# Kernel optimization log

Measured on AMD Instinct MI355X. Metric: run time of the kernel, lower is better.

Reference implementation:

```python
import jax, jax.numpy as jnp
import numpy as np

EMBED = 512
WINDOW = 64

def setup_inputs() -> dict:
    key = jax.random.key(0)
    ks = jax.random.split(key, 5)
    B, S, E = 4, 4096, EMBED
    s = 1.0 / np.sqrt(E)
    x = jax.random.normal(ks[0], (B, S, E), dtype=jnp.float32)
    W_qkv = jax.random.uniform(ks[1], (E, 3 * E), minval=-s, maxval=s, dtype=jnp.float32)
    b_qkv = jax.random.uniform(ks[2], (3 * E,), minval=-s, maxval=s, dtype=jnp.float32)
    W_out = jax.random.uniform(ks[3], (E, E), minval=-s, maxval=s, dtype=jnp.float32)
    b_out = jax.random.uniform(ks[4], (E,), minval=-s, maxval=s, dtype=jnp.float32)
    return {"x": x, "W_qkv": W_qkv, "b_qkv": b_qkv, "W_out": W_out, "b_out": b_out}

def reference(x, W_qkv, b_qkv, W_out, b_out):
    B, S, E = x.shape
    scale = jnp.sqrt(jnp.asarray(E, dtype=x.dtype))
    qkv = x @ W_qkv + b_qkv                    # [B,S,3E]
    q, k, v = jnp.split(qkv, 3, axis=-1)       # each [B,S,E]
    scores = jnp.einsum('bqe,bke->bqk', q, k) / scale  # [B,S,S]
    pos = jnp.arange(S)
    dist = pos[None, :] - pos[:, None]         # [S,S]
    window_mask = jnp.abs(dist) <= WINDOW
    neg_inf = jnp.asarray(-jnp.inf, dtype=scores.dtype)
    scores = jnp.where(window_mask[None, :, :], scores, neg_inf)
    attn = jax.nn.softmax(scores, axis=-1)     # every row has in-window entries
    attended = jnp.einsum('bqk,bke->bqe', attn, v)
    return attended @ W_out + b_out
```

## Files before the change

### kernel.cpp

```cpp
#include <hip/hip_runtime.h>

typedef __attribute__((ext_vector_type(8))) _Float16 f16x8;
typedef __attribute__((ext_vector_type(4))) _Float16 f16x4;
typedef __attribute__((ext_vector_type(4))) float f32x4;
typedef __attribute__((address_space(1))) const char gc_char;
typedef __attribute__((address_space(3))) char ls_char;

#define MFMA(a, b, c) __builtin_amdgcn_mfma_f32_16x16x32_f16((a), (b), (c), 0, 0, 0)
#define FENCE() asm volatile("" ::: "memory")
#define BARRIER() do { FENCE(); __builtin_amdgcn_s_barrier(); FENCE(); } while (0)
#define VMW(n) asm volatile("s_waitcnt vmcnt(" #n ")" ::: "memory")

static constexpr int SEQ = 4096;
static constexpr int EMB = 512;
static constexpr float QSCALE = 0.04419417382415922f;

__device__ __forceinline__ void gl_lds16(const void* g, void* l) {
    __builtin_amdgcn_global_load_lds((gc_char*)g, (ls_char*)l, 16, 0, 0);
}

__global__ void k_prep(const float* __restrict__ x, _Float16* __restrict__ xb,
                       const float* __restrict__ Wq, _Float16* __restrict__ WqT,
                       const float* __restrict__ Wo, _Float16* __restrict__ WoT) {
    const int bid = blockIdx.x, tid = threadIdx.x;
    if (bid < 4096) {
        long i = (long)bid * 256 + tid;
        const float4* p = (const float4*)x + i * 2;
        float4 a = p[0], b = p[1];
        f16x8 v;
        v[0] = (_Float16)a.x; v[1] = (_Float16)a.y; v[2] = (_Float16)a.z; v[3] = (_Float16)a.w;
        v[4] = (_Float16)b.x; v[5] = (_Float16)b.y; v[6] = (_Float16)b.z; v[7] = (_Float16)b.w;
        *(f16x8*)(xb + i * 8) = v;
    } else {
        __shared__ float Ls[64][65];
        int t = bid - 4096;
        const float* W; _Float16* WT; int N, k0, n0;
        if (t < 192) { W = Wq; WT = WqT; N = 1536; k0 = (t & 7) * 64; n0 = (t >> 3) * 64; }
        else { t -= 192; W = Wo; WT = WoT; N = 512; k0 = (t & 7) * 64; n0 = (t >> 3) * 64; }
        int c = tid & 63, r4 = tid >> 6;
#pragma unroll
        for (int i = 0; i < 16; ++i) {
            int row = i * 4 + r4;
            Ls[row][c] = W[(long)(k0 + row) * N + n0 + c];
        }
        __syncthreads();
#pragma unroll
        for (int i = 0; i < 16; ++i) {
            int row = i * 4 + r4;
            WT[(long)(n0 + row) * 512 + k0 + c] = (_Float16)Ls[c][row];
        }
    }
}

template <int NCT, int EPI>
__launch_bounds__(512, 1) __global__
void k_gemm2(const _Float16* __restrict__ A, const _Float16* __restrict__ BT,
             const float* __restrict__ bias, void* o0, void* o1, void* o2) {
    extern __shared__ __align__(16) char smem[];
    const int tid = threadIdx.x, lane = tid & 63, w = tid >> 6, g = lane >> 4, f = lane & 15;
    const int wrow = w >> 2, wcol = w & 3;
    const int bid = blockIdx.x;
    constexpr int NBLK = 128 * NCT;
    const int swz = (bid & 7) * (NBLK / 8) + (bid >> 3);
    const int brow = swz / NCT, bcol = swz - brow * NCT;
    const long row0 = (long)brow * 128;
    const int col0 = bcol * 256;
    const char* Abase = (const char*)A + row0 * 1024;
    const char* Bbase = (const char*)BT + (long)col0 * 1024;

    f32x4 acc[4][4] = {};
    f16x8 a[2][2], breg[2][2][2];

    auto stageA = [&](int h, char* dst, int kt) {
        int rr = tid >> 3;
        int ch = (tid & 7) ^ (rr & 7);
        int grow = h * 32 + (rr & 31) + (rr >> 5) * 64;
        gl_lds16(Abase + (long)grow * 1024 + kt * 128 + ch * 16, dst + h * 8192 + tid * 16);
    };
    auto stageB = [&](int h, char* dst, int kt) {
#pragma unroll
        for (int it = 0; it < 2; ++it) {
            int s = it * 512 + tid;
            int cc = s >> 3;
            int ch = (s & 7) ^ (cc & 7);
            int gcol = h * 32 + (cc & 31) + (cc >> 5) * 64;
            gl_lds16(Bbase + (long)gcol * 1024 + kt * 128 + ch * 16,
                     dst + 16384 + h * 16384 + s * 16);
        }
    };
    auto ldA = [&](const char* buf, int mh) {
#pragma unroll
        for (int mi = 0; mi < 2; ++mi)
#pragma unroll
            for (int ks = 0; ks < 2; ++ks) {
                int rr = wrow * 32 + mi * 16 + f;
                int cl = ks * 4 + g;
                a[mi][ks] = *(const f16x8*)(buf + mh * 8192 + rr * 128 + ((cl ^ (rr & 7)) << 4));
            }
    };
    auto ldB = [&](const char* buf, int nh) {
#pragma unroll
        for (int ni = 0; ni < 2; ++ni)
#pragma unroll
            for (int ks = 0; ks < 2; ++ks) {
                int cc = wcol * 32 + ni * 16 + f;
                int cl = ks * 4 + g;
                breg[nh][ni][ks] =
                    *(const f16x8*)(buf + 16384 + nh * 16384 + cc * 128 + ((cl ^ (cc & 7)) << 4));
            }
    };
    auto mfma8 = [&](int mh, int nh) {
        __builtin_amdgcn_s_setprio(1);
#pragma unroll
        for (int mi = 0; mi < 2; ++mi)
#pragma unroll
            for (int ni = 0; ni < 2; ++ni)
#pragma unroll
                for (int ks = 0; ks < 2; ++ks)
                    acc[mh * 2 + mi][nh * 2 + ni] =
                        MFMA(a[mi][ks], breg[nh][ni][ks], acc[mh * 2 + mi][nh * 2 + ni]);
        __builtin_amdgcn_s_setprio(0);
    };

    stageB(0, smem, 0);
    stageA(0, smem, 0); stageA(1, smem, 0);
    stageB(1, smem, 0);
    VMW(3);
    BARRIER();

    for (int kt = 0; kt < 8; ++kt) {
        const char* cur = smem + (kt & 1) * 49152;
        char* nxt = smem + ((kt + 1) & 1) * 49152;
        const bool last = (kt == 7);
        ldA(cur, 0); ldB(cur, 0);
        if (!last) stageB(0, nxt, kt + 1);
        BARRIER();
        mfma8(0, 0);
        if (!last) { VMW(2); } else { VMW(0); }
        BARRIER();
        ldB(cur, 1);
        if (!last) { stageA(0, nxt, kt + 1); stageA(1, nxt, kt + 1); }
        BARRIER();
        mfma8(0, 1);
        BARRIER();
        ldA(cur, 1);
        if (!last) stageB(1, nxt, kt + 1);
        BARRIER();
        mfma8(1, 0);
        BARRIER();
        mfma8(1, 1);
        if (!last) { VMW(3); }
        BARRIER();
    }

    if (EPI == 1) {
        float* out = (float*)o0;
#pragma unroll
        for (int mi = 0; mi < 4; ++mi)
#pragma unroll
            for (int ni = 0; ni < 4; ++ni) {
                long r0 = row0 + wrow * 64 + mi * 16 + g * 4;
                int c = col0 + wcol * 64 + ni * 16 + f;
                float bv = bias[c];
#pragma unroll
                for (int j = 0; j < 4; ++j)
                    out[(r0 + j) * 512 + c] = acc[mi][ni][j] + bv;
            }
        return;
    }

    float bv[4];
#pragma unroll
    for (int ni = 0; ni < 4; ++ni) bv[ni] = bias[col0 + wcol * 64 + ni * 16 + f];

    if (col0 >= 1024) {
#pragma unroll
        for (int mi = 0; mi < 4; ++mi)
#pragma unroll
            for (int ni = 0; ni < 4; ++ni) {
                int r0 = wrow * 64 + mi * 16 + g * 4;
                int c = wcol * 64 + ni * 16 + f;
                f16x4 v4;
#pragma unroll
                for (int j = 0; j < 4; ++j) v4[j] = (_Float16)(acc[mi][ni][j] + bv[ni]);
                *(f16x4*)(smem + c * 256 + ((r0 * 2) ^ ((c & 7) << 4))) = v4;
            }
        __syncthreads();
        int bb = (int)(row0 >> 12);
        _Float16* vt = (_Float16*)o2 + ((long)bb * 512 + (col0 - 1024)) * 4096 + (row0 & 4095);
#pragma unroll
        for (int it = 0; it < 8; ++it) {
            int slot = it * 512 + tid;
            int e = slot >> 4, ch = slot & 15;
            f16x8 v = *(const f16x8*)(smem + e * 256 + ((ch * 16) ^ ((e & 7) << 4)));
            *(f16x8*)(vt + (long)e * 4096 + ch * 8) = v;
        }
    } else {
        const float sc = (col0 < 512) ? QSCALE : 1.0f;
#pragma unroll
        for (int mi = 0; mi < 4; ++mi)
#pragma unroll
            for (int ni = 0; ni < 4; ++ni)
#pragma unroll
                for (int j = 0; j < 4; ++j) {
                    int r = wrow * 64 + mi * 16 + g * 4 + j;
                    int c = wcol * 64 + ni * 16 + f;
                    float v = (acc[mi][ni][j] + bv[ni]) * sc;
                    int pc = ((c >> 3) + ((r >> 2) & 7) * 2) & 31;
                    *(_Float16*)(smem + r * 512 + pc * 16 + (c & 7) * 2) = (_Float16)v;
                }
        __syncthreads();
        _Float16* dst = (col0 < 512) ? (_Float16*)o0 : (_Float16*)o1;
        int cofs = (col0 < 512) ? col0 : col0 - 512;
#pragma unroll
        for (int it = 0; it < 8; ++it) {
            int slot = it * 512 + tid;
            int r = slot >> 5, ch = slot & 31;
            int pc = (ch + ((r >> 2) & 7) * 2) & 31;
            f16x8 v = *(const f16x8*)(smem + r * 512 + pc * 16);
            *(f16x8*)(dst + (row0 + r) * 512 + cofs + ch * 8) = v;
        }
    }
}

__launch_bounds__(512, 1) __global__
void k_attn(const _Float16* __restrict__ Qb, const _Float16* __restrict__ Kb,
            const _Float16* __restrict__ VT, _Float16* __restrict__ Ob) {
    extern __shared__ __align__(16) char smem[];
    char* buf[2] = { smem, smem + 49152 };
    char* Pl = smem + 98304;
    float* Mp = (float*)(smem + 123904);
    float* Lp = (float*)(smem + 124928);

    const int tid = threadIdx.x, w = tid >> 6, lane = tid & 63, g = lane >> 4, f = lane & 15;
    const int rh = w >> 2, kh = w & 3;
    const int bid = blockIdx.x;
    const int swzb = (bid & 7) * 32 + (bid >> 3);
    const int b = swzb >> 6, qt = swzb & 63;
    const int q0 = qt * 64, kbase = q0 - 64;
    const long bofs = (long)b * SEQ;

    f16x8 qf[2][16];
#pragma unroll
    for (int mt = 0; mt < 2; ++mt) {
        const _Float16* qr = Qb + (bofs + q0 + rh * 32 + mt * 16 + f) * EMB + g * 8;
#pragma unroll
        for (int ks = 0; ks < 16; ++ks) qf[mt][ks] = *(const f16x8*)(qr + ks * 32);
    }

    auto stageK = [&](int ec, char* dst) {
#pragma unroll
        for (int it = 0; it < 6; ++it) {
            int slot = it * 512 + tid;
            int r = slot >> 4, c = slot & 15;
            int cs = c ^ (r & 7);
            int key = min(max(kbase + r, 0), SEQ - 1);
            gl_lds16(Kb + (bofs + key) * EMB + ec * 128 + cs * 8, dst + slot * 16);
        }
    };
    auto stageVT = [&](int ec, char* dst) {
#pragma unroll
        for (int it = 0; it < 6; ++it) {
            int slot = it * 512 + tid;
            int r = slot / 24, c = slot - r * 24;
            int cs = c ^ (r & 7);
            int k0 = min(max(kbase + cs * 8, 0), SEQ - 8);
            gl_lds16(VT + ((long)b * 512 + ec * 128 + r) * 4096 + k0, dst + slot * 16);
        }
    };

    f32x4 sacc[2][3] = {};
    stageK(0, buf[0]);
    __syncthreads();
    for (int ec = 0; ec < 4; ++ec) {
        if (ec < 3) stageK(ec + 1, buf[(ec + 1) & 1]);
        else stageVT(0, buf[0]);
        const char* kb = buf[ec & 1];
#pragma unroll
        for (int kk = 0; kk < 4; ++kk) {
#pragma unroll
            for (int t = 0; t < 3; ++t) {
                int n = kh * 48 + t * 16 + f;
                f16x8 bf = *(const f16x8*)(kb + n * 256 + (((kk * 4 + g) ^ (n & 7)) << 4));
#pragma unroll
                for (int mt = 0; mt < 2; ++mt)
                    sacc[mt][t] = MFMA(qf[mt][ec * 4 + kk], bf, sacc[mt][t]);
            }
        }
        __syncthreads();
    }

    float m[2][4] = {{-3e30f, -3e30f, -3e30f, -3e30f}, {-3e30f, -3e30f, -3e30f, -3e30f}};
    float l[2][4] = {};
#pragma unroll
    for (int mt = 0; mt < 2; ++mt)
#pragma unroll
        for (int t = 0; t < 3; ++t) {
            int key = kbase + kh * 48 + t * 16 + f;
            bool kv = (key >= 0) && (key < SEQ);
#pragma unroll
            for (int j = 0; j < 4; ++j) {
                int d = key - (q0 + rh * 32 + mt * 16 + g * 4 + j);
                bool valid = kv && (d >= -64) && (d <= 64);
                float s = valid ? sacc[mt][t][j] : -3e30f;
                sacc[mt][t][j] = s;
                m[mt][j] = fmaxf(m[mt][j], s);
            }
        }
#pragma unroll
    for (int mt = 0; mt < 2; ++mt)
#pragma unroll
        for (int j = 0; j < 4; ++j) {
            m[mt][j] = fmaxf(m[mt][j], __shfl_xor(m[mt][j], 1));
            m[mt][j] = fmaxf(m[mt][j], __shfl_xor(m[mt][j], 2));
            m[mt][j] = fmaxf(m[mt][j], __shfl_xor(m[mt][j], 4));
            m[mt][j] = fmaxf(m[mt][j], __shfl_xor(m[mt][j], 8));
        }
    if (f == 0) {
#pragma unroll
        for (int mt = 0; mt < 2; ++mt)
#pragma unroll
            for (int j = 0; j < 4; ++j)
                Mp[kh * 64 + rh * 32 + mt * 16 + g * 4 + j] = m[mt][j];
    }
    __syncthreads();
#pragma unroll
    for (int mt = 0; mt < 2; ++mt)
#pragma unroll
        for (int j = 0; j < 4; ++j) {
            int r = rh * 32 + mt * 16 + g * 4 + j;
            m[mt][j] = fmaxf(fmaxf(Mp[r], Mp[64 + r]), fmaxf(Mp[128 + r], Mp[192 + r]));
        }
#pragma unroll
    for (int mt = 0; mt < 2; ++mt)
#pragma unroll
        for (int t = 0; t < 3; ++t)
#pragma unroll
            for (int j = 0; j < 4; ++j) {
                float p = __expf(sacc[mt][t][j] - m[mt][j]);
                sacc[mt][t][j] = p;
                l[mt][j] += p;
            }
#pragma unroll
    for (int mt = 0; mt < 2; ++mt)
#pragma unroll
        for (int j = 0; j < 4; ++j) {
            l[mt][j] += __shfl_xor(l[mt][j], 1);
            l[mt][j] += __shfl_xor(l[mt][j], 2);
            l[mt][j] += __shfl_xor(l[mt][j], 4);
            l[mt][j] += __shfl_xor(l[mt][j], 8);
        }
    if (f == 0) {
#pragma unroll
        for (int mt = 0; mt < 2; ++mt)
#pragma unroll
            for (int j = 0; j < 4; ++j)
                Lp[kh * 64 + rh * 32 + mt * 16 + g * 4 + j] = l[mt][j];
    }
#pragma unroll
    for (int mt = 0; mt < 2; ++mt)
#pragma unroll
        for (int t = 0; t < 3; ++t)
#pragma unroll
            for (int j = 0; j < 4; ++j)
                *(_Float16*)(Pl + (rh * 32 + mt * 16 + g * 4 + j) * 400 +
                             (kh * 48 + t * 16 + f) * 2) = (_Float16)sacc[mt][t][j];
    __syncthreads();

    float rl[2][4];
#pragma unroll
    for (int mt = 0; mt < 2; ++mt)
#pragma unroll
        for (int j = 0; j < 4; ++j) {
            int r = rh * 32 + mt * 16 + g * 4 + j;
            rl[mt][j] = 1.0f / (Lp[r] + Lp[64 + r] + Lp[128 + r] + Lp[192 + r]);
        }

    f16x8 pf[2][6];
#pragma unroll
    for (int mt = 0; mt < 2; ++mt)
#pragma unroll
        for (int kc = 0; kc < 6; ++kc)
            pf[mt][kc] = *(const f16x8*)(Pl + (rh * 32 + mt * 16 + f) * 400 + kc * 64 + g * 16);

    for (int ec = 0; ec < 4; ++ec) {
        if (ec < 3) stageVT(ec + 1, buf[(ec + 1) & 1]);
        const char* vb = buf[ec & 1];
        f32x4 o[2][2] = {};
#pragma unroll
        for (int kc = 0; kc < 6; ++kc) {
#pragma unroll
            for (int nt = 0; nt < 2; ++nt) {
                int e = kh * 32 + nt * 16 + f;
                f16x8 vf = *(const f16x8*)(vb + e * 384 + (((kc * 4 + g) ^ (e & 7)) << 4));
#pragma unroll
                for (int mt = 0; mt < 2; ++mt)
                    o[mt][nt] = MFMA(pf[mt][kc], vf, o[mt][nt]);
            }
        }
#pragma unroll
        for (int mt = 0; mt < 2; ++mt)
#pragma unroll
            for (int nt = 0; nt < 2; ++nt) {
                _Float16* ob = Ob + (bofs + q0 + rh * 32 + mt * 16 + g * 4) * EMB +
                               ec * 128 + kh * 32 + nt * 16 + f;
#pragma unroll
                for (int j = 0; j < 4; ++j)
                    ob[(long)j * EMB] = (_Float16)(o[mt][nt][j] * rl[mt][j]);
            }
        if (ec < 3) __syncthreads();
    }
}

extern "C" void kernel_launch(void* const* d_in, const int* in_sizes, int n_in,
                              void* d_out, int out_size, void* d_ws, size_t ws_size,
                              hipStream_t stream) {
    const float* x     = (const float*)d_in[0];
    const float* W_qkv = (const float*)d_in[1];
    const float* b_qkv = (const float*)d_in[2];
    const float* W_out = (const float*)d_in[3];
    const float* b_out = (const float*)d_in[4];

    char* ws = (char*)d_ws;
    _Float16* xb    = (_Float16*)(ws);
    _Float16* WqkvT = (_Float16*)(ws + 16777216);
    _Float16* WoutT = (_Float16*)(ws + 16777216 + 1572864);
    _Float16* Qb    = (_Float16*)(ws + 18874368);
    _Float16* Kb    = (_Float16*)(ws + 18874368 + 16777216);
    _Float16* VT    = (_Float16*)(ws + 18874368 + 33554432);
    _Float16* Ob    = xb;
    float* out = (float*)d_out;

    (void)hipFuncSetAttribute((const void*)k_gemm2<6, 0>,
                              hipFuncAttributeMaxDynamicSharedMemorySize, 98304);
    (void)hipFuncSetAttribute((const void*)k_gemm2<2, 1>,
                              hipFuncAttributeMaxDynamicSharedMemorySize, 98304);
    (void)hipFuncSetAttribute((const void*)k_attn,
                              hipFuncAttributeMaxDynamicSharedMemorySize, 126976);

    k_prep<<<4352, 256, 0, stream>>>(x, xb, W_qkv, WqkvT, W_out, WoutT);
    k_gemm2<6, 0><<<768, 512, 98304, stream>>>(xb, WqkvT, b_qkv, Qb, Kb, VT);
    k_attn<<<256, 512, 125952, stream>>>(Qb, Kb, VT, Ob);
    k_gemm2<2, 1><<<256, 512, 98304, stream>>>(Ob, WoutT, b_out, out, nullptr, nullptr);
}
```

Baseline: 82.43 us.

## Fuse output projection into attention kernel epilogue

The attention kernel now keeps all four head-dim chunks of the attended output in registers, writes them normalized to LDS as fp16, and runs the output projection GEMM against double-buffered WoutT tiles streamed into LDS. This removes the separate output GEMM launch and the global round trip of the fp16 attention output. In exchange each block holds more accumulator registers, uses a larger shared-memory allocation, and does a serial 64x512x512 GEMM per block with only 256 blocks.

After: 80.50 us. -2.3%, faster.

```diff
diff --git a/kernel.cpp b/kernel.cpp
--- a/kernel.cpp
+++ b/kernel.cpp
@@ -52,17 +52,16 @@
     }
 }
 
-template <int NCT, int EPI>
 __launch_bounds__(512, 1) __global__
-void k_gemm2(const _Float16* __restrict__ A, const _Float16* __restrict__ BT,
-             const float* __restrict__ bias, void* o0, void* o1, void* o2) {
+void k_gemm_qkv(const _Float16* __restrict__ A, const _Float16* __restrict__ BT,
+                const float* __restrict__ bias,
+                _Float16* __restrict__ Qo, _Float16* __restrict__ Ko, _Float16* __restrict__ VT) {
     extern __shared__ __align__(16) char smem[];
     const int tid = threadIdx.x, lane = tid & 63, w = tid >> 6, g = lane >> 4, f = lane & 15;
     const int wrow = w >> 2, wcol = w & 3;
     const int bid = blockIdx.x;
-    constexpr int NBLK = 128 * NCT;
-    const int swz = (bid & 7) * (NBLK / 8) + (bid >> 3);
-    const int brow = swz / NCT, bcol = swz - brow * NCT;
+    const int swz = (bid & 7) * 96 + (bid >> 3);
+    const int brow = swz / 6, bcol = swz - brow * 6;
     const long row0 = (long)brow * 128;
     const int col0 = bcol * 256;
     const char* Abase = (const char*)A + row0 * 1024;
@@ -153,22 +152,6 @@
         BARRIER();
     }
 
-    if (EPI == 1) {
-        float* out = (float*)o0;
-#pragma unroll
-        for (int mi = 0; mi < 4; ++mi)
-#pragma unroll
-            for (int ni = 0; ni < 4; ++ni) {
-                long r0 = row0 + wrow * 64 + mi * 16 + g * 4;
-                int c = col0 + wcol * 64 + ni * 16 + f;
-                float bv = bias[c];
-#pragma unroll
-                for (int j = 0; j < 4; ++j)
-                    out[(r0 + j) * 512 + c] = acc[mi][ni][j] + bv;
-            }
-        return;
-    }
-
     float bv[4];
 #pragma unroll
     for (int ni = 0; ni < 4; ++ni) bv[ni] = bias[col0 + wcol * 64 + ni * 16 + f];
@@ -187,7 +170,7 @@
             }
         __syncthreads();
         int bb = (int)(row0 >> 12);
-        _Float16* vt = (_Float16*)o2 + ((long)bb * 512 + (col0 - 1024)) * 4096 + (row0 & 4095);
+        _Float16* vt = VT + ((long)bb * 512 + (col0 - 1024)) * 4096 + (row0 & 4095);
 #pragma unroll
         for (int it = 0; it < 8; ++it) {
             int slot = it * 512 + tid;
@@ -210,7 +193,7 @@
                     *(_Float16*)(smem + r * 512 + pc * 16 + (c & 7) * 2) = (_Float16)v;
                 }
         __syncthreads();
-        _Float16* dst = (col0 < 512) ? (_Float16*)o0 : (_Float16*)o1;
+        _Float16* dst = (col0 < 512) ? Qo : Ko;
         int cofs = (col0 < 512) ? col0 : col0 - 512;
 #pragma unroll
         for (int it = 0; it < 8; ++it) {
@@ -225,7 +208,8 @@
 
 __launch_bounds__(512, 1) __global__
 void k_attn(const _Float16* __restrict__ Qb, const _Float16* __restrict__ Kb,
-            const _Float16* __restrict__ VT, _Float16* __restrict__ Ob) {
+            const _Float16* __restrict__ VT, const _Float16* __restrict__ WoT,
+            const float* __restrict__ bout, float* __restrict__ Out) {
     extern __shared__ __align__(16) char smem[];
     char* buf[2] = { smem, smem + 49152 };
     char* Pl = smem + 98304;
@@ -383,10 +367,11 @@
         for (int kc = 0; kc < 6; ++kc)
             pf[mt][kc] = *(const f16x8*)(Pl + (rh * 32 + mt * 16 + f) * 400 + kc * 64 + g * 16);
 
+    f32x4 oacc[4][2][2] = {};
+#pragma unroll
     for (int ec = 0; ec < 4; ++ec) {
         if (ec < 3) stageVT(ec + 1, buf[(ec + 1) & 1]);
         const char* vb = buf[ec & 1];
-        f32x4 o[2][2] = {};
 #pragma unroll
         for (int kc = 0; kc < 6; ++kc) {
 #pragma unroll
@@ -395,21 +380,85 @@
                 f16x8 vf = *(const f16x8*)(vb + e * 384 + (((kc * 4 + g) ^ (e & 7)) << 4));
 #pragma unroll
                 for (int mt = 0; mt < 2; ++mt)
-                    o[mt][nt] = MFMA(pf[mt][kc], vf, o[mt][nt]);
-            }
-        }
+                    oacc[ec][mt][nt] = MFMA(pf[mt][kc], vf, oacc[ec][mt][nt]);
+            }
+        }
+        if (ec < 3) __syncthreads();
+    }
+
+    __syncthreads();
+    char* att = smem;
+    char* wb0 = smem + 65536;
+    char* wb1 = smem + 98304;
+
+    auto stageW = [&](int u, char* dst) {
+#pragma unroll
+        for (int i = 0; i < 4; ++i) {
+            int s = i * 512 + tid;
+            int col = s >> 2, ch = s & 3;
+            gl_lds16(WoT + (long)col * 512 + u * 32 + ((ch ^ (col & 3)) * 8), dst + s * 16);
+        }
+    };
+    stageW(0, wb0);
+    stageW(1, wb1);
+#pragma unroll
+    for (int ec = 0; ec < 4; ++ec)
 #pragma unroll
         for (int mt = 0; mt < 2; ++mt)
 #pragma unroll
-            for (int nt = 0; nt < 2; ++nt) {
-                _Float16* ob = Ob + (bofs + q0 + rh * 32 + mt * 16 + g * 4) * EMB +
-                               ec * 128 + kh * 32 + nt * 16 + f;
-#pragma unroll
-                for (int j = 0; j < 4; ++j)
-                    ob[(long)j * EMB] = (_Float16)(o[mt][nt][j] * rl[mt][j]);
-            }
-        if (ec < 3) __syncthreads();
-    }
+            for (int nt = 0; nt < 2; ++nt)
+#pragma unroll
+                for (int j = 0; j < 4; ++j) {
+                    int row = rh * 32 + mt * 16 + g * 4 + j;
+                    int col = ec * 128 + kh * 32 + nt * 16 + f;
+                    *(_Float16*)(att + row * 1024 + ((col * 2) ^ ((row & 7) << 4))) =
+                        (_Float16)(oacc[ec][mt][nt][j] * rl[mt][j]);
+                }
+    __syncthreads();
+
+    float bv2[8];
+#pragma unroll
+    for (int nt = 0; nt < 8; ++nt) bv2[nt] = bout[kh * 128 + nt * 16 + f];
+
+    f32x4 acc2[2][8] = {};
+    for (int u = 0; u < 16; ++u) {
+        const char* wcur = (u & 1) ? wb1 : wb0;
+        f16x8 a2[2];
+#pragma unroll
+        for (int mt = 0; mt < 2; ++mt) {
+            int row = rh * 32 + mt * 16 + f;
+            a2[mt] = *(const f16x8*)(att + row * 1024 + ((u * 64 + g * 16) ^ ((row & 7) << 4)));
+        }
+        __builtin_amdgcn_s_setprio(1);
+#pragma unroll
+        for (int nt = 0; nt < 8; ++nt) {
+            int col = kh * 128 + nt * 16 + f;
+            f16x8 b2 = *(const f16x8*)(wcur + col * 64 + ((g * 16) ^ ((col & 3) << 4)));
+#pragma unroll
+            for (int mt = 0; mt < 2; ++mt)
+                acc2[mt][nt] = MFMA(a2[mt], b2, acc2[mt][nt]);
+        }
+        __builtin_amdgcn_s_setprio(0);
+        BARRIER();
+        if (u + 2 < 16) {
+            stageW(u + 2, (u & 1) ? wb1 : wb0);
+            VMW(4);
+        } else {
+            VMW(0);
+        }
+        BARRIER();
+    }
+
+#pragma unroll
+    for (int mt = 0; mt < 2; ++mt)
+#pragma unroll
+        for (int nt = 0; nt < 8; ++nt) {
+            long r0 = bofs + q0 + rh * 32 + mt * 16 + g * 4;
+            int c = kh * 128 + nt * 16 + f;
+#pragma unroll
+            for (int j = 0; j < 4; ++j)
+                Out[(r0 + j) * 512 + c] = acc2[mt][nt][j] + bv2[nt];
+        }
 }
 
 extern "C" void kernel_launch(void* const* d_in, const int* in_sizes, int n_in,
@@ -428,18 +477,14 @@
     _Float16* Qb    = (_Float16*)(ws + 18874368);
     _Float16* Kb    = (_Float16*)(ws + 18874368 + 16777216);
     _Float16* VT    = (_Float16*)(ws + 18874368 + 33554432);
-    _Float16* Ob    = xb;
     float* out = (float*)d_out;
 
-    (void)hipFuncSetAttribute((const void*)k_gemm2<6, 0>,
-                              hipFuncAttributeMaxDynamicSharedMemorySize, 98304);
-    (void)hipFuncSetAttribute((const void*)k_gemm2<2, 1>,
+    (void)hipFuncSetAttribute((const void*)k_gemm_qkv,
                               hipFuncAttributeMaxDynamicSharedMemorySize, 98304);
     (void)hipFuncSetAttribute((const void*)k_attn,
-                              hipFuncAttributeMaxDynamicSharedMemorySize, 126976);
+                              hipFuncAttributeMaxDynamicSharedMemorySize, 131072);
 
     k_prep<<<4352, 256, 0, stream>>>(x, xb, W_qkv, WqkvT, W_out, WoutT);
-    k_gemm2<6, 0><<<768, 512, 98304, stream>>>(xb, WqkvT, b_qkv, Qb, Kb, VT);
-    k_attn<<<256, 512, 125952, stream>>>(Qb, Kb, VT, Ob);
-    k_gemm2<2, 1><<<256, 512, 98304, stream>>>(Ob, WoutT, b_out, out, nullptr, nullptr);
+    k_gemm_qkv<<<768, 512, 98304, stream>>>(xb, WqkvT, b_qkv, Qb, Kb, VT);
+    k_attn<<<256, 512, 131072, stream>>>(Qb, Kb, VT, WoutT, b_out, out);
 }
```
